# Optimization experiments

Hardware: AMD Instinct MI355X
Metric: run time of the kernel (lower is better)

The kernel has to match this reference:

```python
import jax, jax.numpy as jnp
import numpy as np

B, N, D_OBS, D_NB = 8192, 64, 128, 128
HEADS, GAT_F, GRU_H = 4, 64, 256
ACTION_DIM = 16
PERIOD0 = 24.0
NEG_SLOPE = 0.2
PMAX, PBUDGET = 0.5, 1.0
ENC_DIM = D_OBS + 1  # feature 0 expands to sin/cos
FUSE_IN = ENC_DIM + HEADS * GAT_F


def cyclical_encode(x):
    phase = 2.0 * jnp.pi * x[:, 0] / PERIOD0
    return jnp.concatenate([jnp.sin(phase)[:, None], jnp.cos(phase)[:, None], x[:, 1:]], axis=1)


def gat(node_feat, neigh_feat, mask, W, a):
    # node_feat [B,Din], neigh_feat [B,N,Din], W [Din,H*F], a [H,2F,1]
    b, n, _ = neigh_feat.shape
    h_node = (node_feat @ W).reshape(b, HEADS, GAT_F)            # [B,H,F]
    h_nb = (neigh_feat @ W).reshape(b, n, HEADS, GAT_F)          # [B,N,H,F]
    a_src, a_dst = a[:, :GAT_F, 0], a[:, GAT_F:, 0]              # [H,F] each
    e = (jnp.einsum('bhf,hf->bh', h_node, a_src)[:, None, :]
         + jnp.einsum('bnhf,hf->bnh', h_nb, a_dst))              # [B,N,H]
    e = jnp.where(e > 0, e, NEG_SLOPE * e)                        # leaky_relu
    e = jnp.where(mask[:, :, None], e, -jnp.inf)
    alpha = jax.nn.softmax(e, axis=1)                             # over neighbors
    agg = jnp.einsum('bnh,bnhf->bhf', alpha, h_nb)
    return agg.reshape(b, HEADS * GAT_F)


def gru_cell(x, h, Wih, bih, Whh, bhh):
    gi = x @ Wih + bih
    gh = h @ Whh + bhh
    ir, iz, in_ = jnp.split(gi, 3, axis=-1)
    hr, hz, hn = jnp.split(gh, 3, axis=-1)
    r = jax.nn.sigmoid(ir + hr)
    z = jax.nn.sigmoid(iz + hz)
    nn_ = jnp.tanh(in_ + r * hn)
    return (1.0 - z) * nn_ + z * h


def layer_norm(x, g, b, eps=1e-5):
    mu = jnp.mean(x, axis=-1, keepdims=True)
    var = jnp.var(x, axis=-1, keepdims=True)
    return (x - mu) * jax.lax.rsqrt(var + eps) * g + b


def project_power(raw):
    # Euclidean projection onto {0<=p<=PMAX, sum p<=PBUDGET} via bisection on mu
    def total(mu):
        return jnp.sum(jnp.clip(raw - mu[:, None], 0.0, PMAX), axis=1)
    feas = total(jnp.zeros(raw.shape[0], raw.dtype)) <= PBUDGET
    lo = jnp.zeros(raw.shape[0], raw.dtype)
    hi = jnp.maximum(jnp.max(raw, axis=1), 0.0)
    def body(_, lh):
        lo, hi = lh
        mid = 0.5 * (lo + hi)
        over = total(mid) > PBUDGET
        return (jnp.where(over, mid, lo), jnp.where(over, hi, mid))
    lo, hi = jax.lax.fori_loop(0, 60, body, (lo, hi))
    mu = jnp.where(feas, 0.0, hi)
    return jnp.clip(raw - mu[:, None], 0.0, PMAX)


def setup_inputs() -> dict:
    key = jax.random.key(0)
    ks = jax.random.split(key, 20)
    def init(k, shape, fan_in):
        return (jax.random.normal(k, shape, jnp.float32) / np.sqrt(fan_in)).astype(jnp.float32)
    mask = jax.random.bernoulli(ks[3], 0.5, (B, N))
    mask = mask.at[:, 0].set(True)  # guarantee >=1 valid neighbor per row
    return {
        'node_obs': jax.random.normal(ks[0], (B, D_OBS), jnp.float32),
        'neighbor_obs': jax.random.normal(ks[1], (B, N, D_NB), jnp.float32),
        'neighbor_mask': mask,
        'hidden_state': jnp.zeros((1, B, GRU_H), jnp.float32),
        'W_gat': init(ks[4], (D_NB, HEADS * GAT_F), D_NB),
        'a_gat': init(ks[5], (HEADS, 2 * GAT_F, 1), 2 * GAT_F),
        'fusion_W': init(ks[6], (FUSE_IN, GRU_H), FUSE_IN),
        'fusion_b': jnp.zeros((GRU_H,), jnp.float32),
        'Wih': init(ks[7], (GRU_H, 3 * GRU_H), GRU_H),
        'bih': jnp.zeros((3 * GRU_H,), jnp.float32),
        'Whh': init(ks[8], (GRU_H, 3 * GRU_H), GRU_H),
        'bhh': jnp.zeros((3 * GRU_H,), jnp.float32),
        'ln_g': jnp.ones((GRU_H,), jnp.float32),
        'ln_b': jnp.zeros((GRU_H,), jnp.float32),
        'W1': init(ks[9], (GRU_H, 256), GRU_H),
        'b1': jnp.zeros((256,), jnp.float32),
        'W2': init(ks[10], (256, 128), 256),
        'b2': jnp.zeros((128,), jnp.float32),
        'W3': init(ks[11], (128, ACTION_DIM), 128),
        'b3': jnp.zeros((ACTION_DIM,), jnp.float32),
    }


def reference(node_obs, neighbor_obs, neighbor_mask, hidden_state,
              W_gat, a_gat, fusion_W, fusion_b, Wih, bih, Whh, bhh,
              ln_g, ln_b, W1, b1, W2, b2, W3, b3):
    enc = cyclical_encode(node_obs)                              # [B, ENC_DIM]
    node_feat_for_gat = neighbor_obs[:, 0, :]
    ctx = gat(node_feat_for_gat, neighbor_obs, neighbor_mask, W_gat, a_gat)
    fused = jax.nn.relu(jnp.concatenate([enc, ctx], axis=-1) @ fusion_W + fusion_b)
    h_new = gru_cell(fused, hidden_state[0], Wih, bih, Whh, bhh)  # 1-step GRU
    belief = layer_norm(h_new, ln_g, ln_b)
    x = jax.nn.relu(belief @ W1 + b1)
    x = jax.nn.relu(x @ W2 + b2)
    raw = x @ W3 + b3                                            # [B, ACTION_DIM]
    action = project_power(raw)
    return action, h_new[None, :, :]
```

## Files before the change

### kernel.cpp

```cpp
#include <hip/hip_runtime.h>
#include <hip/hip_bf16.h>


typedef unsigned short u16;
typedef unsigned int   u32;
typedef __attribute__((ext_vector_type(8))) short bf16x8;
typedef __attribute__((ext_vector_type(4))) float f32x4;

#define KFUSE  672
#define ACT_TOT (8192*16)

__device__ __forceinline__ u16 f2bf(float x){
  u32 u = __float_as_uint(x);
  u += 0x7fffu + ((u >> 16) & 1u);
  return (u16)(u >> 16);
}
__device__ __forceinline__ float bf2f(u16 h){ return __uint_as_float(((u32)h) << 16); }

__device__ __forceinline__ void frag_one(const float* __restrict__ src, int ld, int col0,
                                         int NT, u16* __restrict__ dhi, u16* __restrict__ dlo,
                                         int f, int fsrc, int l){
  int kt = fsrc / NT, nt = fsrc % NT;
  int kbase = kt*32 + (l >> 4)*8, n = col0 + nt*16 + (l & 15);
  size_t o = ((size_t)f*64 + l)*8;
  #pragma unroll
  for(int i = 0; i < 8; ++i){
    float w = src[(size_t)(kbase + i)*ld + n];
    u16 h = f2bf(w);
    dhi[o + i] = h;
    dlo[o + i] = f2bf(w - bf2f(h));
  }
}

#define B_WBIG0 1
#define B_WRZA  673
#define B_WRZB  737
#define B_WIN   801
#define B_WHN   833
#define B_F1    865
#define B_F2    897
#define B_SPLIT 913
__global__ __launch_bounds__(256) void k_prep1(
    const unsigned char* __restrict__ maskb, int* __restrict__ flag,
    const float* __restrict__ Wg, const float* __restrict__ ag,
    float* __restrict__ was, float* __restrict__ wad,
    const float* __restrict__ fW, float* __restrict__ wbig,
    const float* __restrict__ Wih, const float* __restrict__ Whh,
    const float* __restrict__ W1, const float* __restrict__ W2,
    u16* __restrict__ wrzh, u16* __restrict__ wrzl,
    u16* __restrict__ winh, u16* __restrict__ winl,
    u16* __restrict__ whnh, u16* __restrict__ whnl,
    u16* __restrict__ f1h, u16* __restrict__ f1l,
    u16* __restrict__ f2h, u16* __restrict__ f2l,
    const float* __restrict__ hidden, u16* __restrict__ acath, u16* __restrict__ acatl)
{
  int bx = blockIdx.x, t = threadIdx.x;
  if(bx == 0){
    if(t == 0){
      int s = 0;
      for(int i = 1; i < 256; i += 4) s += maskb[i];
      *flag = (s == 0) ? 1 : 0;
    }
    #pragma unroll
    for(int v = 0; v < 2; ++v){
      int idx = v*256 + t, k = idx & 127, h = idx >> 7;
      float s = 0.f, d = 0.f;
      for(int f = 0; f < 64; ++f){
        float w = Wg[k*256 + h*64 + f];
        s += w * ag[h*128 + f];
        d += w * ag[h*128 + 64 + f];
      }
      was[k*4 + h] = s; wad[k*4 + h] = d;
    }
  } else if(bx < B_WRZA){
    int r = bx - B_WBIG0, j = t;
    float v;
    if(r < 129) v = fW[r*256 + j];
    else if(r < 641){
      int h = (r - 129) >> 7, kk = (r - 129) & 127;
      float s = 0.f;
      for(int f = 0; f < 64; ++f) s += Wg[kk*256 + h*64 + f] * fW[(129 + h*64 + f)*256 + j];
      v = s;
    } else v = 0.f;
    wbig[r*256 + j] = v;
  } else if(bx < B_SPLIT){
    int sub = t >> 6, l = t & 63;
    if(bx < B_WRZB){
      int f = (bx - B_WRZA)*4 + sub;
      frag_one(Wih, 768, 0, 32, wrzh, wrzl, f, f, l);
    } else if(bx < B_WIN){
      int fl = (bx - B_WRZB)*4 + sub;
      frag_one(Whh, 768, 0, 32, wrzh, wrzl, 256 + fl, fl, l);
    } else if(bx < B_WHN){
      int f = (bx - B_WIN)*4 + sub;
      frag_one(Wih, 768, 512, 16, winh, winl, f, f, l);
    } else if(bx < B_F1){
      int f = (bx - B_WHN)*4 + sub;
      frag_one(Whh, 768, 512, 16, whnh, whnl, f, f, l);
    } else if(bx < B_F2){
      int f = (bx - B_F1)*4 + sub;
      frag_one(W1, 256, 0, 16, f1h, f1l, f, f, l);
    } else {
      int f = (bx - B_F2)*4 + sub;
      frag_one(W2, 128, 0, 8, f2h, f2l, f, f, l);
    }
  } else {
    int i = (bx - B_SPLIT)*256 + t;
    int idx8 = i*8, row = idx8 >> 8, col = idx8 & 255;
    const float4* p = (const float4*)(hidden + (size_t)idx8);
    float4 v0 = p[0], v1 = p[1];
    float vv[8] = {v0.x,v0.y,v0.z,v0.w,v1.x,v1.y,v1.z,v1.w};
    u16 h8[8], l8[8];
    #pragma unroll
    for(int q = 0; q < 8; ++q){ u16 h = f2bf(vv[q]); h8[q] = h; l8[q] = f2bf(vv[q] - bf2f(h)); }
    uint4 uh = { (u32)h8[0] | ((u32)h8[1]<<16), (u32)h8[2] | ((u32)h8[3]<<16),
                 (u32)h8[4] | ((u32)h8[5]<<16), (u32)h8[6] | ((u32)h8[7]<<16) };
    uint4 ul = { (u32)l8[0] | ((u32)l8[1]<<16), (u32)l8[2] | ((u32)l8[3]<<16),
                 (u32)l8[4] | ((u32)l8[5]<<16), (u32)l8[6] | ((u32)l8[7]<<16) };
    size_t off = (size_t)row*512 + 256 + col;
    *(uint4*)(acath + off) = uh;
    *(uint4*)(acatl + off) = ul;
  }
}

__global__ __launch_bounds__(256) void k_prep2(
    const float* __restrict__ wbig, u16* __restrict__ ffh, u16* __restrict__ ffl)
{
  int f = blockIdx.x*4 + (threadIdx.x >> 6), l = threadIdx.x & 63;
  frag_one(wbig, 256, 0, 16, ffh, ffl, f, f, l);
}

__global__ __launch_bounds__(256) void k_gat(
    const float* __restrict__ nbg, const float* __restrict__ node,
    const void* __restrict__ maskp, const int* __restrict__ flagp,
    const float* __restrict__ was, const float* __restrict__ wad,
    u16* __restrict__ xhi, u16* __restrict__ xlo)
{
  __shared__ float s_nb[8192];
  __shared__ float s_wad[512];
  __shared__ float s_ep[1024];
  __shared__ float s_alpha[256];
  int b = blockIdx.x, t = threadIdx.x;
  const float* nb = nbg + (size_t)b*8192;
  const int isint = *flagp;

  s_wad[t] = wad[t]; s_wad[t+256] = wad[t+256];

  #pragma unroll
  for(int q = 0; q < 8; ++q){
    int f = q*256 + t;
    int n = f >> 5, ch = f & 31;
    float4 v = *(const float4*)(nb + f*4);
    *(float4*)(s_nb + (n*32 + (ch ^ (n & 31)))*4) = v;
  }

  if(t < 129){
    float v;
    if(t < 2){
      float ph = node[(size_t)b*128] * (6.2831853071795864769f / 24.0f);
      v = (t == 0) ? sinf(ph) : cosf(ph);
    } else v = node[(size_t)b*128 + (t-1)];
    u16 h = f2bf(v);
    size_t o = (size_t)b*KFUSE + t;
    xhi[o] = h; xlo[o] = f2bf(v - bf2f(h));
  } else if(t < 160){
    size_t o = (size_t)b*KFUSE + 641 + (t - 129);
    xhi[o] = 0; xlo[o] = 0;
  }
  __syncthreads();

  {
    int n = t & 63, c = t >> 6;
    float adx = 0.f, ady = 0.f, adz = 0.f, adw = 0.f;
    #pragma unroll
    for(int q = 0; q < 8; ++q){
      int ch = c*8 + q;
      float4 v = *(const float4*)(s_nb + (n*32 + (ch ^ (n & 31)))*4);
      float vv[4] = {v.x, v.y, v.z, v.w};
      #pragma unroll
      for(int i2 = 0; i2 < 4; ++i2){
        int k = ch*4 + i2;
        float4 wd = *(const float4*)(s_wad + k*4);
        adx += vv[i2]*wd.x; ady += vv[i2]*wd.y; adz += vv[i2]*wd.z; adw += vv[i2]*wd.w;
      }
    }
    float4 ad = {adx, ady, adz, adw};
    *(float4*)(s_ep + (c*64 + n)*4) = ad;
  }
  __syncthreads();

  {
    int n2 = t & 63, h2 = t >> 6;
    float es = 0.f;
    #pragma unroll
    for(int ii = 0; ii < 2; ++ii){
      int k = n2*2 + ii;
      float v0 = s_nb[(k >> 2)*4 + (k & 3)];
      es += v0 * was[k*4 + h2];
    }
    for(int off = 32; off; off >>= 1) es += __shfl_xor(es, off);
    float ed = s_ep[n2*4 + h2] + s_ep[(64+n2)*4 + h2]
             + s_ep[(128+n2)*4 + h2] + s_ep[(192+n2)*4 + h2];
    float e = es + ed;
    e = (e > 0.f) ? e : 0.2f*e;
    bool valid;
    if(isint) valid = ((const u32*)maskp)[(size_t)b*64 + n2] != 0u;
    else      valid = ((const unsigned char*)maskp)[(size_t)b*64 + n2] != 0;
    float ev = valid ? e : -1e30f;
    float m = ev;
    for(int off = 32; off; off >>= 1) m = fmaxf(m, __shfl_xor(m, off));
    float p = valid ? expf(ev - m) : 0.f;
    float s = p;
    for(int off = 32; off; off >>= 1) s += __shfl_xor(s, off);
    s_alpha[n2*4 + h2] = p / s;
  }
  __syncthreads();

  {
    int c2 = t & 31, hp = (t >> 6) & 1, half = t >> 7;
    int sub = (t >> 5) & 1;
    float4 a0 = {0.f,0.f,0.f,0.f}, a1 = {0.f,0.f,0.f,0.f};
    int nbase = half*32 + sub*16;
    #pragma unroll
    for(int i = 0; i < 16; ++i){
      int n = nbase + i;
      float4 v = *(const float4*)(s_nb + (n*32 + (c2 ^ (n & 31)))*4);
      float2 ap = *(const float2*)(s_alpha + n*4 + hp*2);
      a0.x += ap.x*v.x; a0.y += ap.x*v.y; a0.z += ap.x*v.z; a0.w += ap.x*v.w;
      a1.x += ap.y*v.x; a1.y += ap.y*v.y; a1.z += ap.y*v.z; a1.w += ap.y*v.w;
    }
    a0.x += __shfl_xor(a0.x, 32); a0.y += __shfl_xor(a0.y, 32);
    a0.z += __shfl_xor(a0.z, 32); a0.w += __shfl_xor(a0.w, 32);
    a1.x += __shfl_xor(a1.x, 32); a1.y += __shfl_xor(a1.y, 32);
    a1.z += __shfl_xor(a1.z, 32); a1.w += __shfl_xor(a1.w, 32);
    __syncthreads();
    if((t & 63) < 32){
      int w = t >> 6;
      *(float4*)(s_ep + (w*32 + c2)*8 + 0) = a0;
      *(float4*)(s_ep + (w*32 + c2)*8 + 4) = a1;
    }
  }
  __syncthreads();
  if(t < 128){
    int h = t >> 5, cc = t & 31;
    int hp2 = h >> 1, slot = h & 1;
    float4 p0 = *(const float4*)(s_ep + ((0*2 + hp2)*32 + cc)*8 + slot*4);
    float4 p1 = *(const float4*)(s_ep + ((1*2 + hp2)*32 + cc)*8 + slot*4);
    float vv[4] = {p0.x+p1.x, p0.y+p1.y, p0.z+p1.z, p0.w+p1.w};
    size_t o = (size_t)b*KFUSE + 129 + h*128 + cc*4;
    #pragma unroll
    for(int i = 0; i < 4; ++i){
      u16 hh = f2bf(vv[i]);
      xhi[o+i] = hh; xlo[o+i] = f2bf(vv[i] - bf2f(hh));
    }
  }
}

template<int KT, int NT_TOT, int NPW, int ROWF>
__global__ __launch_bounds__(256) void k_gemm3(
    const u16* __restrict__ xhi, const u16* __restrict__ xlo, int lda,
    const u16* __restrict__ wfhi, const u16* __restrict__ wflo,
    const float* __restrict__ bias,
    u16* __restrict__ ohi, u16* __restrict__ olo, int ost, int ocol)
{
  int l = threadIdx.x & 63, w = threadIdx.x >> 6;
  int m0 = blockIdx.x * (16*ROWF);
  int ntbase = blockIdx.y * (4*NPW) + w*NPW;
  f32x4 acc[NPW][ROWF];
  #pragma unroll
  for(int j = 0; j < NPW; ++j)
    #pragma unroll
    for(int rf = 0; rf < ROWF; ++rf) acc[j][rf] = (f32x4){0.f,0.f,0.f,0.f};
  size_t arow[ROWF];
  #pragma unroll
  for(int rf = 0; rf < ROWF; ++rf)
    arow[rf] = (size_t)(m0 + rf*16 + (l & 15))*lda + (size_t)((l >> 4)*8);
  bf16x8 ah[ROWF], al[ROWF];
  #pragma unroll
  for(int rf = 0; rf < ROWF; ++rf){
    ah[rf] = *(const bf16x8*)(xhi + arow[rf]);
    al[rf] = *(const bf16x8*)(xlo + arow[rf]);
  }
  for(int kt = 0; kt < KT; ++kt){
    bf16x8 ahn[ROWF], aln[ROWF];
    if(kt + 1 < KT){
      #pragma unroll
      for(int rf = 0; rf < ROWF; ++rf){
        ahn[rf] = *(const bf16x8*)(xhi + arow[rf] + (kt+1)*32);
        aln[rf] = *(const bf16x8*)(xlo + arow[rf] + (kt+1)*32);
      }
    }
    #pragma unroll
    for(int j = 0; j < NPW; ++j){
      size_t bo = ((size_t)(kt*NT_TOT + ntbase + j)*64 + l)*8;
      bf16x8 bh = *(const bf16x8*)(wfhi + bo);
      bf16x8 bl = *(const bf16x8*)(wflo + bo);
      #pragma unroll
      for(int rf = 0; rf < ROWF; ++rf){
        acc[j][rf] = __builtin_amdgcn_mfma_f32_16x16x32_bf16(ah[rf], bh, acc[j][rf], 0, 0, 0);
        acc[j][rf] = __builtin_amdgcn_mfma_f32_16x16x32_bf16(ah[rf], bl, acc[j][rf], 0, 0, 0);
        acc[j][rf] = __builtin_amdgcn_mfma_f32_16x16x32_bf16(al[rf], bh, acc[j][rf], 0, 0, 0);
      }
    }
    #pragma unroll
    for(int rf = 0; rf < ROWF; ++rf){ ah[rf] = ahn[rf]; al[rf] = aln[rf]; }
  }
  #pragma unroll
  for(int j = 0; j < NPW; ++j){
    int col = (ntbase + j)*16 + (l & 15);
    float bv = bias[col];
    #pragma unroll
    for(int rf = 0; rf < ROWF; ++rf){
      int r0 = m0 + rf*16 + (l >> 4)*4;
      #pragma unroll
      for(int q = 0; q < 4; ++q){
        float y = fmaxf(acc[j][rf][q] + bv, 0.f);
        size_t o = (size_t)(r0 + q)*ost + ocol + col;
        u16 h = f2bf(y);
        ohi[o] = h; olo[o] = f2bf(y - bf2f(h));
      }
    }
  }
}

__global__ __launch_bounds__(512) void k_gru(
    const u16* __restrict__ ah_, const u16* __restrict__ al_,
    const u16* __restrict__ wrzh, const u16* __restrict__ wrzl,
    const u16* __restrict__ winh, const u16* __restrict__ winl,
    const u16* __restrict__ whnh, const u16* __restrict__ whnl,
    const float* __restrict__ bih, const float* __restrict__ bhh,
    const float* __restrict__ hidden, const float* __restrict__ lng,
    const float* __restrict__ lnb,
    float* __restrict__ hout, u16* __restrict__ belh, u16* __restrict__ bell)
{
  __shared__ float s_s1[256], s_s2[256];
  __shared__ float s_mu[32], s_rs[32];
  int l = threadIdx.x & 63, w = threadIdx.x >> 6;
  int m0 = blockIdx.x*32;
  f32x4 ar[2][2], az[2][2], aa[2][2], ab[2][2];
  #pragma unroll
  for(int j = 0; j < 2; ++j)
    #pragma unroll
    for(int rf = 0; rf < 2; ++rf){
      ar[j][rf] = (f32x4){0.f,0.f,0.f,0.f}; az[j][rf] = (f32x4){0.f,0.f,0.f,0.f};
      aa[j][rf] = (f32x4){0.f,0.f,0.f,0.f}; ab[j][rf] = (f32x4){0.f,0.f,0.f,0.f};
    }
  size_t arow[2];
  #pragma unroll
  for(int rf = 0; rf < 2; ++rf)
    arow[rf] = (size_t)(m0 + rf*16 + (l & 15))*512 + (size_t)((l >> 4)*8);
  for(int kt = 0; kt < 16; ++kt){
    bf16x8 ah[2], al[2];
    #pragma unroll
    for(int rf = 0; rf < 2; ++rf){
      ah[rf] = *(const bf16x8*)(ah_ + arow[rf] + kt*32);
      al[rf] = *(const bf16x8*)(al_ + arow[rf] + kt*32);
    }
    #pragma unroll
    for(int j = 0; j < 2; ++j){
      int nt = w*2 + j;
      int fr = kt*32 + nt;
      size_t bo = ((size_t)fr*64 + l)*8;
      bf16x8 bh = *(const bf16x8*)(wrzh + bo);
      bf16x8 bl = *(const bf16x8*)(wrzl + bo);
      size_t bo2 = bo + (size_t)16*64*8;
      bf16x8 bh2 = *(const bf16x8*)(wrzh + bo2);
      bf16x8 bl2 = *(const bf16x8*)(wrzl + bo2);
      #pragma unroll
      for(int rf = 0; rf < 2; ++rf){
        ar[j][rf] = __builtin_amdgcn_mfma_f32_16x16x32_bf16(ah[rf], bh, ar[j][rf], 0, 0, 0);
        ar[j][rf] = __builtin_amdgcn_mfma_f32_16x16x32_bf16(ah[rf], bl, ar[j][rf], 0, 0, 0);
        ar[j][rf] = __builtin_amdgcn_mfma_f32_16x16x32_bf16(al[rf], bh, ar[j][rf], 0, 0, 0);
        az[j][rf] = __builtin_amdgcn_mfma_f32_16x16x32_bf16(ah[rf], bh2, az[j][rf], 0, 0, 0);
        az[j][rf] = __builtin_amdgcn_mfma_f32_16x16x32_bf16(ah[rf], bl2, az[j][rf], 0, 0, 0);
        az[j][rf] = __builtin_amdgcn_mfma_f32_16x16x32_bf16(al[rf], bh2, az[j][rf], 0, 0, 0);
      }
    }
  }
  for(int kt = 0; kt < 8; ++kt){
    bf16x8 fh[2], fl2[2], gh[2], gl[2];
    #pragma unroll
    for(int rf = 0; rf < 2; ++rf){
      fh[rf]  = *(const bf16x8*)(ah_ + arow[rf] + kt*32);
      fl2[rf] = *(const bf16x8*)(al_ + arow[rf] + kt*32);
      gh[rf]  = *(const bf16x8*)(ah_ + arow[rf] + 256 + kt*32);
      gl[rf]  = *(const bf16x8*)(al_ + arow[rf] + 256 + kt*32);
    }
    #pragma unroll
    for(int j = 0; j < 2; ++j){
      int nt = w*2 + j;
      size_t bo = ((size_t)(kt*16 + nt)*64 + l)*8;
      bf16x8 bh = *(const bf16x8*)(winh + bo);
      bf16x8 bl = *(const bf16x8*)(winl + bo);
      bf16x8 ch = *(const bf16x8*)(whnh + bo);
      bf16x8 cl2 = *(const bf16x8*)(whnl + bo);
      #pragma unroll
      for(int rf = 0; rf < 2; ++rf){
        aa[j][rf] = __builtin_amdgcn_mfma_f32_16x16x32_bf16(fh[rf], bh, aa[j][rf], 0, 0, 0);
        aa[j][rf] = __builtin_amdgcn_mfma_f32_16x16x32_bf16(fh[rf], bl, aa[j][rf], 0, 0, 0);
        aa[j][rf] = __builtin_amdgcn_mfma_f32_16x16x32_bf16(fl2[rf], bh, aa[j][rf], 0, 0, 0);
        ab[j][rf] = __builtin_amdgcn_mfma_f32_16x16x32_bf16(gh[rf], ch, ab[j][rf], 0, 0, 0);
        ab[j][rf] = __builtin_amdgcn_mfma_f32_16x16x32_bf16(gh[rf], cl2, ab[j][rf], 0, 0, 0);
        ab[j][rf] = __builtin_amdgcn_mfma_f32_16x16x32_bf16(gl[rf], ch, ab[j][rf], 0, 0, 0);
      }
    }
  }
  int cl = l & 15, rq = l >> 4;
  float hnew[2][2][4];
  float s1p[2][4], s2p[2][4];
  #pragma unroll
  for(int rf = 0; rf < 2; ++rf)
    #pragma unroll
    for(int q = 0; q < 4; ++q){ s1p[rf][q] = 0.f; s2p[rf][q] = 0.f; }
  #pragma unroll
  for(int j = 0; j < 2; ++j){
    int col = w*32 + j*16 + cl;
    float br = bih[col] + bhh[col];
    float bz = bih[256+col] + bhh[256+col];
    float bi = bih[512+col];
    float bh2 = bhh[512+col];
    #pragma unroll
    for(int rf = 0; rf < 2; ++rf){
      #pragma unroll
      for(int q = 0; q < 4; ++q){
        int row = m0 + rf*16 + rq*4 + q;
        float rs = ar[j][rf][q] + br;
        float zs = az[j][rf][q] + bz;
        float in_ = aa[j][rf][q] + bi;
        float hn  = ab[j][rf][q] + bh2;
        float h   = hidden[(size_t)row*256 + col];
        float r = 1.f/(1.f + expf(-rs));
        float z = 1.f/(1.f + expf(-zs));
        float nv = tanhf(in_ + r*hn);
        float hv = (1.f - z)*nv + z*h;
        hnew[j][rf][q] = hv;
        hout[(size_t)row*256 + col] = hv;
        s1p[rf][q] += hv; s2p[rf][q] += hv*hv;
      }
    }
  }
  #pragma unroll
  for(int rf = 0; rf < 2; ++rf)
    #pragma unroll
    for(int q = 0; q < 4; ++q){
      float a = s1p[rf][q], b2 = s2p[rf][q];
      for(int off = 1; off < 16; off <<= 1){
        a += __shfl_xor(a, off); b2 += __shfl_xor(b2, off);
      }
      if(cl == 0){
        int rloc = rf*16 + rq*4 + q;
        s_s1[w*32 + rloc] = a; s_s2[w*32 + rloc] = b2;
      }
    }
  __syncthreads();
  if(threadIdx.x < 32){
    int rloc = threadIdx.x;
    float t1 = 0.f, t2 = 0.f;
    #pragma unroll
    for(int ww = 0; ww < 8; ++ww){ t1 += s_s1[ww*32 + rloc]; t2 += s_s2[ww*32 + rloc]; }
    float mu = t1 * (1.f/256.f);
    float var = t2 * (1.f/256.f) - mu*mu;
    s_mu[rloc] = mu; s_rs[rloc] = rsqrtf(var + 1e-5f);
  }
  __syncthreads();
  #pragma unroll
  for(int j = 0; j < 2; ++j){
    int col = w*32 + j*16 + cl;
    float g = lng[col], bb = lnb[col];
    #pragma unroll
    for(int rf = 0; rf < 2; ++rf){
      #pragma unroll
      for(int q = 0; q < 4; ++q){
        int rloc = rf*16 + rq*4 + q;
        float bel = (hnew[j][rf][q] - s_mu[rloc]) * s_rs[rloc] * g + bb;
        u16 hb = f2bf(bel);
        size_t o = (size_t)(m0 + rloc)*256 + col;
        belh[o] = hb; bell[o] = f2bf(bel - bf2f(hb));
      }
    }
  }
}

__global__ __launch_bounds__(256) void k_w2head(
    const u16* __restrict__ xhi, const u16* __restrict__ xlo,
    const u16* __restrict__ wfhi, const u16* __restrict__ wflo,
    const float* __restrict__ b2, const float* __restrict__ W3,
    const float* __restrict__ b3, float* __restrict__ act)
{
  __shared__ float sx2[32*128];
  __shared__ float sW3[2048];
  int t = threadIdx.x, l = t & 63, w = t >> 6;
  int m0 = blockIdx.x*32;
  for(int i = t; i < 2048; i += 256) sW3[i] = W3[i];
  f32x4 acc[2][2];
  #pragma unroll
  for(int j = 0; j < 2; ++j)
    #pragma unroll
    for(int rf = 0; rf < 2; ++rf) acc[j][rf] = (f32x4){0.f,0.f,0.f,0.f};
  size_t arow[2];
  #pragma unroll
  for(int rf = 0; rf < 2; ++rf)
    arow[rf] = (size_t)(m0 + rf*16 + (l & 15))*256 + (size_t)((l >> 4)*8);
  for(int kt = 0; kt < 8; ++kt){
    bf16x8 ah[2], al[2];
    #pragma unroll
    for(int rf = 0; rf < 2; ++rf){
      ah[rf] = *(const bf16x8*)(xhi + arow[rf] + kt*32);
      al[rf] = *(const bf16x8*)(xlo + arow[rf] + kt*32);
    }
    #pragma unroll
    for(int j = 0; j < 2; ++j){
      size_t bo = ((size_t)(kt*8 + w*2 + j)*64 + l)*8;
      bf16x8 bh = *(const bf16x8*)(wfhi + bo);
      bf16x8 bl = *(const bf16x8*)(wflo + bo);
      #pragma unroll
      for(int rf = 0; rf < 2; ++rf){
        acc[j][rf] = __builtin_amdgcn_mfma_f32_16x16x32_bf16(ah[rf], bh, acc[j][rf], 0, 0, 0);
        acc[j][rf] = __builtin_amdgcn_mfma_f32_16x16x32_bf16(ah[rf], bl, acc[j][rf], 0, 0, 0);
        acc[j][rf] = __builtin_amdgcn_mfma_f32_16x16x32_bf16(al[rf], bh, acc[j][rf], 0, 0, 0);
      }
    }
  }
  int cl = l & 15, rq = l >> 4;
  #pragma unroll
  for(int j = 0; j < 2; ++j){
    int col = (w*2 + j)*16 + cl;
    float bv = b2[col];
    #pragma unroll
    for(int rf = 0; rf < 2; ++rf){
      #pragma unroll
      for(int q = 0; q < 4; ++q){
        int rloc = rf*16 + rq*4 + q;
        sx2[rloc*128 + col] = fmaxf(acc[j][rf][q] + bv, 0.f);
      }
    }
  }
  __syncthreads();
  int j = t & 15, rl = t >> 4;
  #pragma unroll
  for(int rr = 0; rr < 2; ++rr){
    int rloc = rr*16 + rl;
    const float* xr = sx2 + rloc*128;
    float raw = b3[j];
    #pragma unroll 8
    for(int k4 = 0; k4 < 32; ++k4){
      float4 v = *(const float4*)(xr + k4*4);
      raw += v.x*sW3[(k4*4+0)*16 + j] + v.y*sW3[(k4*4+1)*16 + j]
           + v.z*sW3[(k4*4+2)*16 + j] + v.w*sW3[(k4*4+3)*16 + j];
    }
    float c0 = fminf(fmaxf(raw, 0.f), 0.5f);
    float tot = c0;
    for(int off = 8; off; off >>= 1) tot += __shfl_xor(tot, off);
    float mx = raw;
    for(int off = 8; off; off >>= 1) mx = fmaxf(mx, __shfl_xor(mx, off));
    bool feas = (tot <= 1.0f);
    float lo = 0.f, hi = fmaxf(mx, 0.f);
    for(int it = 0; it < 60; ++it){
      float mid = 0.5f*(lo + hi);
      float s = fminf(fmaxf(raw - mid, 0.f), 0.5f);
      for(int off = 8; off; off >>= 1) s += __shfl_xor(s, off);
      bool over = s > 1.0f;
      lo = over ? mid : lo;
      hi = over ? hi : mid;
    }
    float muv = feas ? 0.f : hi;
    act[(size_t)(m0 + rloc)*16 + j] = fminf(fmaxf(raw - muv, 0.f), 0.5f);
  }
}

#define OFF_FLAG   0u
#define OFF_WAS    4096u
#define OFF_WAD    8192u
#define OFF_WBIG   12288u
#define OFF_FFH    700416u
#define OFF_FFL    1044480u
#define OFF_WRZH   1388544u
#define OFF_WRZL   1912832u
#define OFF_WINH   2437120u
#define OFF_WINL   2568192u
#define OFF_WHNH   2699264u
#define OFF_WHNL   2830336u
#define OFF_F1H    2961408u
#define OFF_F1L    3092480u
#define OFF_F2H    3223552u
#define OFF_F2L    3289088u
#define OFF_XCATH  3354624u
#define OFF_XCATL  14364672u
#define OFF_ACATH  25374720u
#define OFF_ACATL  33763328u
#define OFF_BELH   42151936u
#define OFF_BELL   46346240u
#define OFF_X1H    50540544u
#define OFF_X1L    54734848u

extern "C" void kernel_launch(void* const* d_in, const int* in_sizes, int n_in,
                              void* d_out, int out_size, void* d_ws, size_t ws_size,
                              hipStream_t stream){
  const float* node   = (const float*)d_in[0];
  const float* nbr    = (const float*)d_in[1];
  const void*  mask   = d_in[2];
  const float* hidden = (const float*)d_in[3];
  const float* Wg     = (const float*)d_in[4];
  const float* ag     = (const float*)d_in[5];
  const float* fW     = (const float*)d_in[6];
  const float* fb     = (const float*)d_in[7];
  const float* Wih    = (const float*)d_in[8];
  const float* bih    = (const float*)d_in[9];
  const float* Whh    = (const float*)d_in[10];
  const float* bhh    = (const float*)d_in[11];
  const float* lng    = (const float*)d_in[12];
  const float* lnb    = (const float*)d_in[13];
  const float* W1     = (const float*)d_in[14];
  const float* b1     = (const float*)d_in[15];
  const float* W2     = (const float*)d_in[16];
  const float* b2     = (const float*)d_in[17];
  const float* W3     = (const float*)d_in[18];
  const float* b3     = (const float*)d_in[19];
  char* ws = (char*)d_ws;
  float* out = (float*)d_out;

  int*   flag = (int*)  (ws + OFF_FLAG);
  float* was  = (float*)(ws + OFF_WAS);
  float* wad  = (float*)(ws + OFF_WAD);
  float* wbig = (float*)(ws + OFF_WBIG);
  u16* ffh  = (u16*)(ws + OFF_FFH);   u16* ffl  = (u16*)(ws + OFF_FFL);
  u16* wrzh = (u16*)(ws + OFF_WRZH);  u16* wrzl = (u16*)(ws + OFF_WRZL);
  u16* winh = (u16*)(ws + OFF_WINH);  u16* winl = (u16*)(ws + OFF_WINL);
  u16* whnh = (u16*)(ws + OFF_WHNH);  u16* whnl = (u16*)(ws + OFF_WHNL);
  u16* f1h  = (u16*)(ws + OFF_F1H);   u16* f1l  = (u16*)(ws + OFF_F1L);
  u16* f2h  = (u16*)(ws + OFF_F2H);   u16* f2l  = (u16*)(ws + OFF_F2L);
  u16* xh   = (u16*)(ws + OFF_XCATH); u16* xl   = (u16*)(ws + OFF_XCATL);
  u16* ach  = (u16*)(ws + OFF_ACATH); u16* acl  = (u16*)(ws + OFF_ACATL);
  u16* beh  = (u16*)(ws + OFF_BELH);  u16* bel  = (u16*)(ws + OFF_BELL);
  u16* x1h  = (u16*)(ws + OFF_X1H);   u16* x1l  = (u16*)(ws + OFF_X1L);

  k_prep1<<<1937, 256, 0, stream>>>((const unsigned char*)mask, flag, Wg, ag, was, wad,
                                    fW, wbig, Wih, Whh, W1, W2,
                                    wrzh, wrzl, winh, winl, whnh, whnl,
                                    f1h, f1l, f2h, f2l, hidden, ach, acl);
  k_prep2<<<84, 256, 0, stream>>>(wbig, ffh, ffl);

  k_gat<<<8192, 256, 0, stream>>>(nbr, node, mask, flag, was, wad, xh, xl);

  k_gemm3<21,16,2,4><<<dim3(128,2), 256, 0, stream>>>(xh, xl, KFUSE, ffh, ffl, fb, ach, acl, 512, 0);
  k_gru<<<256, 512, 0, stream>>>(ach, acl, wrzh, wrzl, winh, winl, whnh, whnl,
                                 bih, bhh, hidden, lng, lnb, out + ACT_TOT, beh, bel);
  k_gemm3<8,16,2,4><<<dim3(128,2), 256, 0, stream>>>(beh, bel, 256, f1h, f1l, b1, x1h, x1l, 256, 0);
  k_w2head<<<256, 256, 0, stream>>>(x1h, x1l, f2h, f2l, b2, W3, b3, out);
}
```

Before: 192.1 us.

## Process eight GAT rows per block with register prefetch of next row

The GAT kernel now handles 8 batch rows per block instead of one, and launches 1024 blocks instead of 8192. While the current row is computed out of shared memory, the next row's 32KB of neighbor features is prefetched into registers. The block barrier is replaced by a custom one that waits only on LDS counters, so the global prefetch loads can stay in flight across barriers. The aim is to hide HBM latency and cut per-block launch and tail cost, at the price of more registers and fewer resident blocks available to hide latency.

```diff
diff --git a/kernel.cpp b/kernel.cpp
--- a/kernel.cpp
+++ b/kernel.cpp
@@ -9,6 +9,7 @@
 
 #define KFUSE  672
 #define ACT_TOT (8192*16)
+#define GAT_ROWS 8
 
 __device__ __forceinline__ u16 f2bf(float x){
   u32 u = __float_as_uint(x);
@@ -16,6 +17,12 @@
   return (u16)(u >> 16);
 }
 __device__ __forceinline__ float bf2f(u16 h){ return __uint_as_float(((u32)h) << 16); }
+
+__device__ __forceinline__ void gbar(){
+  asm volatile("s_waitcnt lgkmcnt(0)" ::: "memory");
+  __builtin_amdgcn_s_barrier();
+  __builtin_amdgcn_sched_barrier(0);
+}
 
 __device__ __forceinline__ void frag_one(const float* __restrict__ src, int ld, int col0,
                                          int NT, u16* __restrict__ dhi, u16* __restrict__ dlo,
@@ -140,118 +147,135 @@
   __shared__ float s_wad[512];
   __shared__ float s_ep[1024];
   __shared__ float s_alpha[256];
-  int b = blockIdx.x, t = threadIdx.x;
-  const float* nb = nbg + (size_t)b*8192;
+  int t = threadIdx.x;
   const int isint = *flagp;
+  int b0 = blockIdx.x * GAT_ROWS;
 
   s_wad[t] = wad[t]; s_wad[t+256] = wad[t+256];
 
-  #pragma unroll
-  for(int q = 0; q < 8; ++q){
-    int f = q*256 + t;
-    int n = f >> 5, ch = f & 31;
-    float4 v = *(const float4*)(nb + f*4);
-    *(float4*)(s_nb + (n*32 + (ch ^ (n & 31)))*4) = v;
-  }
-
-  if(t < 129){
-    float v;
-    if(t < 2){
-      float ph = node[(size_t)b*128] * (6.2831853071795864769f / 24.0f);
-      v = (t == 0) ? sinf(ph) : cosf(ph);
-    } else v = node[(size_t)b*128 + (t-1)];
-    u16 h = f2bf(v);
-    size_t o = (size_t)b*KFUSE + t;
-    xhi[o] = h; xlo[o] = f2bf(v - bf2f(h));
-  } else if(t < 160){
-    size_t o = (size_t)b*KFUSE + 641 + (t - 129);
-    xhi[o] = 0; xlo[o] = 0;
-  }
-  __syncthreads();
-
+  float4 pf[8];
   {
-    int n = t & 63, c = t >> 6;
-    float adx = 0.f, ady = 0.f, adz = 0.f, adw = 0.f;
+    const float* nb = nbg + (size_t)b0*8192;
+    #pragma unroll
+    for(int q = 0; q < 8; ++q)
+      pf[q] = *(const float4*)(nb + (size_t)(q*256 + t)*4);
+  }
+
+  for(int r = 0; r < GAT_ROWS; ++r){
+    int b = b0 + r;
     #pragma unroll
     for(int q = 0; q < 8; ++q){
-      int ch = c*8 + q;
-      float4 v = *(const float4*)(s_nb + (n*32 + (ch ^ (n & 31)))*4);
-      float vv[4] = {v.x, v.y, v.z, v.w};
-      #pragma unroll
-      for(int i2 = 0; i2 < 4; ++i2){
-        int k = ch*4 + i2;
-        float4 wd = *(const float4*)(s_wad + k*4);
-        adx += vv[i2]*wd.x; ady += vv[i2]*wd.y; adz += vv[i2]*wd.z; adw += vv[i2]*wd.w;
-      }
-    }
-    float4 ad = {adx, ady, adz, adw};
-    *(float4*)(s_ep + (c*64 + n)*4) = ad;
-  }
-  __syncthreads();
-
-  {
-    int n2 = t & 63, h2 = t >> 6;
-    float es = 0.f;
-    #pragma unroll
-    for(int ii = 0; ii < 2; ++ii){
-      int k = n2*2 + ii;
-      float v0 = s_nb[(k >> 2)*4 + (k & 3)];
-      es += v0 * was[k*4 + h2];
-    }
-    for(int off = 32; off; off >>= 1) es += __shfl_xor(es, off);
-    float ed = s_ep[n2*4 + h2] + s_ep[(64+n2)*4 + h2]
-             + s_ep[(128+n2)*4 + h2] + s_ep[(192+n2)*4 + h2];
-    float e = es + ed;
-    e = (e > 0.f) ? e : 0.2f*e;
-    bool valid;
-    if(isint) valid = ((const u32*)maskp)[(size_t)b*64 + n2] != 0u;
-    else      valid = ((const unsigned char*)maskp)[(size_t)b*64 + n2] != 0;
-    float ev = valid ? e : -1e30f;
-    float m = ev;
-    for(int off = 32; off; off >>= 1) m = fmaxf(m, __shfl_xor(m, off));
-    float p = valid ? expf(ev - m) : 0.f;
-    float s = p;
-    for(int off = 32; off; off >>= 1) s += __shfl_xor(s, off);
-    s_alpha[n2*4 + h2] = p / s;
-  }
-  __syncthreads();
-
-  {
-    int c2 = t & 31, hp = (t >> 6) & 1, half = t >> 7;
-    int sub = (t >> 5) & 1;
-    float4 a0 = {0.f,0.f,0.f,0.f}, a1 = {0.f,0.f,0.f,0.f};
-    int nbase = half*32 + sub*16;
-    #pragma unroll
-    for(int i = 0; i < 16; ++i){
-      int n = nbase + i;
-      float4 v = *(const float4*)(s_nb + (n*32 + (c2 ^ (n & 31)))*4);
-      float2 ap = *(const float2*)(s_alpha + n*4 + hp*2);
-      a0.x += ap.x*v.x; a0.y += ap.x*v.y; a0.z += ap.x*v.z; a0.w += ap.x*v.w;
-      a1.x += ap.y*v.x; a1.y += ap.y*v.y; a1.z += ap.y*v.z; a1.w += ap.y*v.w;
-    }
-    a0.x += __shfl_xor(a0.x, 32); a0.y += __shfl_xor(a0.y, 32);
-    a0.z += __shfl_xor(a0.z, 32); a0.w += __shfl_xor(a0.w, 32);
-    a1.x += __shfl_xor(a1.x, 32); a1.y += __shfl_xor(a1.y, 32);
-    a1.z += __shfl_xor(a1.z, 32); a1.w += __shfl_xor(a1.w, 32);
-    __syncthreads();
-    if((t & 63) < 32){
-      int w = t >> 6;
-      *(float4*)(s_ep + (w*32 + c2)*8 + 0) = a0;
-      *(float4*)(s_ep + (w*32 + c2)*8 + 4) = a1;
-    }
-  }
-  __syncthreads();
-  if(t < 128){
-    int h = t >> 5, cc = t & 31;
-    int hp2 = h >> 1, slot = h & 1;
-    float4 p0 = *(const float4*)(s_ep + ((0*2 + hp2)*32 + cc)*8 + slot*4);
-    float4 p1 = *(const float4*)(s_ep + ((1*2 + hp2)*32 + cc)*8 + slot*4);
-    float vv[4] = {p0.x+p1.x, p0.y+p1.y, p0.z+p1.z, p0.w+p1.w};
-    size_t o = (size_t)b*KFUSE + 129 + h*128 + cc*4;
-    #pragma unroll
-    for(int i = 0; i < 4; ++i){
-      u16 hh = f2bf(vv[i]);
-      xhi[o+i] = hh; xlo[o+i] = f2bf(vv[i] - bf2f(hh));
+      int f = q*256 + t;
+      int n = f >> 5, ch = f & 31;
+      *(float4*)(s_nb + (n*32 + (ch ^ (n & 31)))*4) = pf[q];
+    }
+    gbar();
+
+    if(r + 1 < GAT_ROWS){
+      const float* nb = nbg + (size_t)(b+1)*8192;
+      #pragma unroll
+      for(int q = 0; q < 8; ++q)
+        pf[q] = *(const float4*)(nb + (size_t)(q*256 + t)*4);
+    }
+
+    if(t < 129){
+      float v;
+      if(t < 2){
+        float ph = node[(size_t)b*128] * (6.2831853071795864769f / 24.0f);
+        v = (t == 0) ? sinf(ph) : cosf(ph);
+      } else v = node[(size_t)b*128 + (t-1)];
+      u16 h = f2bf(v);
+      size_t o = (size_t)b*KFUSE + t;
+      xhi[o] = h; xlo[o] = f2bf(v - bf2f(h));
+    } else if(t < 160){
+      size_t o = (size_t)b*KFUSE + 641 + (t - 129);
+      xhi[o] = 0; xlo[o] = 0;
+    }
+
+    {
+      int n = t & 63, c = t >> 6;
+      float adx = 0.f, ady = 0.f, adz = 0.f, adw = 0.f;
+      #pragma unroll
+      for(int q = 0; q < 8; ++q){
+        int ch = c*8 + q;
+        float4 v = *(const float4*)(s_nb + (n*32 + (ch ^ (n & 31)))*4);
+        float vv[4] = {v.x, v.y, v.z, v.w};
+        #pragma unroll
+        for(int i2 = 0; i2 < 4; ++i2){
+          int k = ch*4 + i2;
+          float4 wd = *(const float4*)(s_wad + k*4);
+          adx += vv[i2]*wd.x; ady += vv[i2]*wd.y; adz += vv[i2]*wd.z; adw += vv[i2]*wd.w;
+        }
+      }
+      float4 ad = {adx, ady, adz, adw};
+      *(float4*)(s_ep + (c*64 + n)*4) = ad;
+    }
+    gbar();
+
+    {
+      int n2 = t & 63, h2 = t >> 6;
+      float es = 0.f;
+      #pragma unroll
+      for(int ii = 0; ii < 2; ++ii){
+        int k = n2*2 + ii;
+        float v0 = s_nb[(k >> 2)*4 + (k & 3)];
+        es += v0 * was[k*4 + h2];
+      }
+      for(int off = 32; off; off >>= 1) es += __shfl_xor(es, off);
+      float ed = s_ep[n2*4 + h2] + s_ep[(64+n2)*4 + h2]
+               + s_ep[(128+n2)*4 + h2] + s_ep[(192+n2)*4 + h2];
+      float e = es + ed;
+      e = (e > 0.f) ? e : 0.2f*e;
+      bool valid;
+      if(isint) valid = ((const u32*)maskp)[(size_t)b*64 + n2] != 0u;
+      else      valid = ((const unsigned char*)maskp)[(size_t)b*64 + n2] != 0;
+      float ev = valid ? e : -1e30f;
+      float m = ev;
+      for(int off = 32; off; off >>= 1) m = fmaxf(m, __shfl_xor(m, off));
+      float p = valid ? expf(ev - m) : 0.f;
+      float s = p;
+      for(int off = 32; off; off >>= 1) s += __shfl_xor(s, off);
+      s_alpha[n2*4 + h2] = p / s;
+    }
+    gbar();
+
+    {
+      int c2 = t & 31, hp = (t >> 6) & 1, half = t >> 7;
+      int sub = (t >> 5) & 1;
+      float4 a0 = {0.f,0.f,0.f,0.f}, a1 = {0.f,0.f,0.f,0.f};
+      int nbase = half*32 + sub*16;
+      #pragma unroll
+      for(int i = 0; i < 16; ++i){
+        int n = nbase + i;
+        float4 v = *(const float4*)(s_nb + (n*32 + (c2 ^ (n & 31)))*4);
+        float2 ap = *(const float2*)(s_alpha + n*4 + hp*2);
+        a0.x += ap.x*v.x; a0.y += ap.x*v.y; a0.z += ap.x*v.z; a0.w += ap.x*v.w;
+        a1.x += ap.y*v.x; a1.y += ap.y*v.y; a1.z += ap.y*v.z; a1.w += ap.y*v.w;
+      }
+      a0.x += __shfl_xor(a0.x, 32); a0.y += __shfl_xor(a0.y, 32);
+      a0.z += __shfl_xor(a0.z, 32); a0.w += __shfl_xor(a0.w, 32);
+      a1.x += __shfl_xor(a1.x, 32); a1.y += __shfl_xor(a1.y, 32);
+      a1.z += __shfl_xor(a1.z, 32); a1.w += __shfl_xor(a1.w, 32);
+      gbar();
+      if((t & 63) < 32){
+        int w = t >> 6;
+        *(float4*)(s_ep + (w*32 + c2)*8 + 0) = a0;
+        *(float4*)(s_ep + (w*32 + c2)*8 + 4) = a1;
+      }
+    }
+    gbar();
+    if(t < 128){
+      int h = t >> 5, cc = t & 31;
+      int hp2 = h >> 1, slot = h & 1;
+      float4 p0 = *(const float4*)(s_ep + ((0*2 + hp2)*32 + cc)*8 + slot*4);
+      float4 p1 = *(const float4*)(s_ep + ((1*2 + hp2)*32 + cc)*8 + slot*4);
+      float vv[4] = {p0.x+p1.x, p0.y+p1.y, p0.z+p1.z, p0.w+p1.w};
+      size_t o = (size_t)b*KFUSE + 129 + h*128 + cc*4;
+      #pragma unroll
+      for(int i = 0; i < 4; ++i){
+        u16 hh = f2bf(vv[i]);
+        xhi[o+i] = hh; xlo[o+i] = f2bf(vv[i] - bf2f(hh));
+      }
     }
   }
 }
@@ -640,7 +664,7 @@
                                     f1h, f1l, f2h, f2l, hidden, ach, acl);
   k_prep2<<<84, 256, 0, stream>>>(wbig, ffh, ffl);
 
-  k_gat<<<8192, 256, 0, stream>>>(nbr, node, mask, flag, was, wad, xh, xl);
+  k_gat<<<1024, 256, 0, stream>>>(nbr, node, mask, flag, was, wad, xh, xl);
 
   k_gemm3<21,16,2,4><<<dim3(128,2), 256, 0, stream>>>(xh, xl, KFUSE, ffh, ffl, fb, ach, acl, 512, 0);
   k_gru<<<256, 512, 0, stream>>>(ach, acl, wrzh, wrzl, winh, winl, whnh, whnl,
```

Measured after the change: 284.8 us. 1.48x slower.
